# Kernel tuning notes

Hardware: AMD Instinct MI355X
Metric: run time of the kernel (lower is better)

## Reference

```python
import jax, jax.numpy as jnp
import numpy as np

BOARD_H, BOARD_W = 10, 9
NUM_NODES = BOARD_H * BOARD_W  # 90
NUM_HEADS = 4


def _build_base_adjacency():
    adj = np.zeros((NUM_NODES, NUM_NODES), dtype=np.float32)
    for y in range(BOARD_H):
        for x in range(BOARD_W):
            idx = y * BOARD_W + x
            for dy, dx in [(0, 1), (0, -1), (1, 0), (-1, 0)]:
                ny, nx = y + dy, x + dx
                if 0 <= ny < BOARD_H and 0 <= nx < BOARD_W:
                    adj[idx, ny * BOARD_W + nx] = 1.0
            for nx in range(BOARD_W):
                if nx != x and abs(nx - x) <= 4:
                    nidx = y * BOARD_W + nx
                    adj[idx, nidx] = max(adj[idx, nidx], 1.0 / abs(nx - x))
            for ny in range(BOARD_H):
                if ny != y and abs(ny - y) <= 5:
                    nidx = ny * BOARD_W + x
                    adj[idx, nidx] = max(adj[idx, nidx], 1.0 / abs(ny - y))
            adj[idx, idx] = 1.0
    deg = np.clip(adj.sum(-1, keepdims=True), 1.0, None)
    return adj / deg  # (90, 90)


def _pos_encoding():
    px = (np.arange(BOARD_W, dtype=np.float32) / BOARD_W)
    py = (np.arange(BOARD_H, dtype=np.float32) / BOARD_H)
    gx = np.broadcast_to(px[None, :], (BOARD_H, BOARD_W)).reshape(-1)
    gy = np.broadcast_to(py[:, None], (BOARD_H, BOARD_W)).reshape(-1)
    return np.stack([gx, gy], axis=-1)  # (90, 2)


def _gat_layer(x, adj, W, a_src, a_dst, gamma, beta):
    B, N, _ = x.shape
    h = (x @ W).reshape(B, N, NUM_HEADS, -1)          # (B,N,H,D)
    s_src = jnp.einsum('bnhd,hd->bhn', h, a_src)       # (B,H,N)
    s_dst = jnp.einsum('bnhd,hd->bhn', h, a_dst)
    attn = s_src[..., :, None] + s_dst[..., None, :]   # (B,H,N,N)
    attn = jax.nn.leaky_relu(attn, 0.2)
    attn = jnp.where((adj == 0)[None, None], -jnp.inf, attn)
    attn = jax.nn.softmax(attn, axis=-1)
    attn = jnp.nan_to_num(attn, nan=0.0)
    out = jnp.einsum('bhij,bjhd->bihd', attn, h).reshape(B * N, -1)
    # BatchNorm1d in training mode: biased batch stats over (B*N)
    mean = out.mean(0)
    var = out.var(0)
    out = (out - mean) * jax.lax.rsqrt(var + 1e-5) * gamma + beta
    return jax.nn.relu(out.reshape(B, N, -1))


def setup_inputs() -> dict:
    key = jax.random.key(0)
    ks = jax.random.split(key, 16)
    B, F_in, Hd, Dout = 2048, 16, 64, 128
    hdim = Hd // NUM_HEADS
    p = lambda k, s: (jax.random.normal(k, s, dtype=jnp.float32) * 0.1)
    return {
        'board_planes': jax.random.uniform(ks[0], (B, 14, BOARD_H, BOARD_W), dtype=jnp.float32),
        'in_W': p(ks[1], (F_in, Hd)), 'in_b': p(ks[2], (Hd,)),
        'W0': p(ks[3], (Hd, Hd)), 'asrc0': p(ks[4], (NUM_HEADS, hdim)), 'adst0': p(ks[5], (NUM_HEADS, hdim)),
        'g0': jnp.ones((Hd,), jnp.float32), 'b0': jnp.zeros((Hd,), jnp.float32),
        'W1': p(ks[6], (Hd, Hd)), 'asrc1': p(ks[7], (NUM_HEADS, hdim)), 'adst1': p(ks[8], (NUM_HEADS, hdim)),
        'g1': jnp.ones((Hd,), jnp.float32), 'b1': jnp.zeros((Hd,), jnp.float32),
        'out_W': p(ks[9], (Hd, Dout)), 'out_b': p(ks[10], (Dout,)),
    }


def reference(board_planes, in_W, in_b, W0, asrc0, adst0, g0, b0,
              W1, asrc1, adst1, g1, b1, out_W, out_b):
    B = board_planes.shape[0]
    adj = jnp.asarray(_build_base_adjacency())            # (90,90), same for all batches
    nodes = board_planes.reshape(B, 14, NUM_NODES).transpose(0, 2, 1)  # (B,90,14)
    pos = jnp.broadcast_to(jnp.asarray(_pos_encoding())[None], (B, NUM_NODES, 2))
    x = jnp.concatenate([nodes, pos], axis=-1)            # (B,90,16)
    x = x @ in_W + in_b
    x = _gat_layer(x, adj, W0, asrc0, adst0, g0, b0)
    x = _gat_layer(x, adj, W1, asrc1, adst1, g1, b1)
    return x.mean(axis=1) @ out_W + out_b                 # (B,128)
```

## Files before the change

### kernel.cpp

```cpp
#include <hip/hip_runtime.h>
#include <cstdint>


#define BB   2048
#define NN   90
#define NP   96
#define CC   64
#define NH   4
#define HD   16
#define TPB  512
#define DOUT 128
#define SXP  72
#define SWP  72
#define SHP  68
#define PPITCH 20
#define NSLOT 19

typedef _Float16 f16;
typedef _Float16 f16x4 __attribute__((ext_vector_type(4)));
typedef _Float16 f16x8 __attribute__((ext_vector_type(8)));
typedef float f32x4 __attribute__((ext_vector_type(4)));
union U16x4 { f16x4 v; f16 e[4]; };

#define LDS_BYTES 40832

template <int LAYER>
__global__ __launch_bounds__(TPB, 8) void k_gat(
    const float* __restrict__ bp,
    const float* __restrict__ inW,
    const float* __restrict__ inb,
    const float* __restrict__ prevPre,
    const float* __restrict__ stPrev,
    const float* __restrict__ Wl,
    const float* __restrict__ asrc,
    const float* __restrict__ adst,
    float* __restrict__ outPre,
    float* __restrict__ partial,
    float* __restrict__ partialSq)
{
    __shared__ __align__(16) unsigned char lds[LDS_BYTES];
    float* shF  = (float*)lds;
    f16*   sx   = (f16*)lds;
    f16*   sWt  = (f16*)(lds + 13824);
    unsigned char* uni = lds + 24480;
    f16*   sXr  = (f16*)uni;
    float* sInW = (float*)(uni + 3072);
    float* sInb = (float*)(uni + 7168);
    float* sAs  = (float*)(uni + 7424);
    float* sAd  = (float*)(uni + 7680);
    f16*   sPh  = (f16*)uni;
    float* sRa  = (float*)uni;
    float* sRb  = (float*)(uni + 2048);
    f16*   sSrcH = (f16*)(lds + 38880);
    f16*   sDstH = (f16*)(lds + 39600);
    float* sST   = (float*)(lds + 40320);

    const int b = blockIdx.x, t = threadIdx.x;
    const int cq = t & 15, ng = t >> 4;
    const int c4 = cq << 2;
    const int jcnt = (ng < NN - 64) ? 3 : 2;
    const int lane = t & 63, wv = t >> 6;
    const int lr = lane & 15, lg = lane >> 4;

    for (int i = t; i < CC * CC; i += TPB) {
        int k = i >> 6, c = i & 63;
        sWt[c * SWP + k] = (f16)Wl[i];
    }
    if (t < NH * HD) { sAs[t] = asrc[t]; sAd[t] = adst[t]; }
    if (t < (NP - NN) * (SXP / 4)) {
        int r = t / (SXP / 4), q = t - r * (SXP / 4);
        f16x4 z = {(f16)0, (f16)0, (f16)0, (f16)0};
        *(f16x4*)&sx[(NN + r) * SXP + q * 4] = z;
    }
    if (LAYER == 0) {
        for (int i = t; i < 16 * CC; i += TPB) sInW[i] = inW[i];
        if (t < CC) sInb[t] = inb[t];
        const float* bpb = bp + (size_t)b * (14 * NN);
        for (int i = t; i < 14 * NN; i += TPB) {
            int p = i / NN, n = i - p * NN;
            sXr[n * 17 + p] = (f16)bpb[i];
        }
        if (t < NN) {
            int y = t / 9, x = t - y * 9;
            sXr[t * 17 + 14] = (f16)((float)x / 9.0f);
            sXr[t * 17 + 15] = (f16)((float)y / 10.0f);
        }
    } else {
        if (t < 2 * CC) sST[t] = stPrev[t];
    }
    __syncthreads();

    if (LAYER == 0) {
        const int n0 = ng, n1 = ng + 32, n2 = (jcnt == 3) ? ng + 64 : ng;
        float acc[3][4] = {};
        #pragma unroll 4
        for (int k = 0; k < 16; k++) {
            float4 w = *(const float4*)&sInW[k * CC + c4];
            float x0 = (float)sXr[n0 * 17 + k];
            float x1 = (float)sXr[n1 * 17 + k];
            float x2 = (float)sXr[n2 * 17 + k];
            acc[0][0] = fmaf(x0, w.x, acc[0][0]); acc[0][1] = fmaf(x0, w.y, acc[0][1]);
            acc[0][2] = fmaf(x0, w.z, acc[0][2]); acc[0][3] = fmaf(x0, w.w, acc[0][3]);
            acc[1][0] = fmaf(x1, w.x, acc[1][0]); acc[1][1] = fmaf(x1, w.y, acc[1][1]);
            acc[1][2] = fmaf(x1, w.z, acc[1][2]); acc[1][3] = fmaf(x1, w.w, acc[1][3]);
            acc[2][0] = fmaf(x2, w.x, acc[2][0]); acc[2][1] = fmaf(x2, w.y, acc[2][1]);
            acc[2][2] = fmaf(x2, w.z, acc[2][2]); acc[2][3] = fmaf(x2, w.w, acc[2][3]);
        }
        float4 bias = *(const float4*)&sInb[c4];
        for (int j = 0; j < jcnt; j++) {
            int n = ng + 32 * j;
            f16x4 o;
            o.x = (f16)(acc[j][0] + bias.x);
            o.y = (f16)(acc[j][1] + bias.y);
            o.z = (f16)(acc[j][2] + bias.z);
            o.w = (f16)(acc[j][3] + bias.w);
            *(f16x4*)&sx[n * SXP + c4] = o;
        }
    } else {
        const float4* pv4 = (const float4*)(prevPre + (size_t)b * (NN * CC));
        for (int i4 = t; i4 < NN * CC / 4; i4 += TPB) {
            float4 v = pv4[i4];
            int n = i4 >> 4, c = (i4 & 15) << 2;
            float a0 = fmaf(v.x, sST[c + 0], sST[CC + c + 0]);
            float a1 = fmaf(v.y, sST[c + 1], sST[CC + c + 1]);
            float a2 = fmaf(v.z, sST[c + 2], sST[CC + c + 2]);
            float a3 = fmaf(v.w, sST[c + 3], sST[CC + c + 3]);
            f16x4 o;
            o.x = (f16)(a0 > 0.0f ? a0 : 0.0f);
            o.y = (f16)(a1 > 0.0f ? a1 : 0.0f);
            o.z = (f16)(a2 > 0.0f ? a2 : 0.0f);
            o.w = (f16)(a3 > 0.0f ? a3 : 0.0f);
            *(f16x4*)&sx[n * SXP + c] = o;
        }
    }
    __syncthreads();

    {
        const int nt = wv & 3, m0 = wv >> 2;
        const f16x8 bf0 = *(const f16x8*)&sWt[(nt * 16 + lr) * SWP + lg * 8];
        const f16x8 bf1 = *(const f16x8*)&sWt[(nt * 16 + lr) * SWP + 32 + lg * 8];
        f16x8 af0[3], af1[3];
        #pragma unroll
        for (int mi = 0; mi < 3; mi++) {
            const int mt = m0 + 2 * mi;
            af0[mi] = *(const f16x8*)&sx[(mt * 16 + lr) * SXP + lg * 8];
            af1[mi] = *(const f16x8*)&sx[(mt * 16 + lr) * SXP + 32 + lg * 8];
        }
        __syncthreads();
        #pragma unroll
        for (int mi = 0; mi < 3; mi++) {
            const int mt = m0 + 2 * mi;
            f32x4 acc = {0.0f, 0.0f, 0.0f, 0.0f};
            acc = __builtin_amdgcn_mfma_f32_16x16x32_f16(af0[mi], bf0, acc, 0, 0, 0);
            acc = __builtin_amdgcn_mfma_f32_16x16x32_f16(af1[mi], bf1, acc, 0, 0, 0);
            const int row = mt * 16 + lg * 4, col = nt * 16 + lr;
            #pragma unroll
            for (int r = 0; r < 4; r++)
                if (row + r < NN) shF[(row + r) * SHP + col] = acc[r];
        }
    }
    __syncthreads();

    if (t < NH * NN) {
        int hh = t / NN, n = t - hh * NN;
        const float4* hv = (const float4*)&shF[n * SHP + hh * HD];
        const float4* av = (const float4*)&sAs[hh * HD];
        const float4* dv = (const float4*)&sAd[hh * HD];
        float a = 0.0f, d = 0.0f;
        #pragma unroll
        for (int m = 0; m < 4; m++) {
            float4 h4 = hv[m], am = av[m], dm = dv[m];
            a = fmaf(h4.x, am.x, a); a = fmaf(h4.y, am.y, a);
            a = fmaf(h4.z, am.z, a); a = fmaf(h4.w, am.w, a);
            d = fmaf(h4.x, dm.x, d); d = fmaf(h4.y, dm.y, d);
            d = fmaf(h4.z, dm.z, d); d = fmaf(h4.w, dm.w, d);
        }
        sSrcH[t] = (f16)a; sDstH[t] = (f16)d;
    }
    __syncthreads();

    if (t < NH * NN) {
        int hh = t / NN, n = t - hh * NN;
        int y = n / 9, x = n - y * 9;
        float si = (float)sSrcH[t];
        float e[NSLOT];
        #pragma unroll
        for (int xx = 0; xx < 9; xx++) {
            int dx = xx > x ? xx - x : x - xx;
            float ee = si + (float)sDstH[hh * NN + y * 9 + xx];
            ee = ee > 0.0f ? ee : 0.2f * ee;
            e[xx] = (dx <= 4) ? ee : -1e30f;
        }
        #pragma unroll
        for (int yy = 0; yy < 10; yy++) {
            int dy = yy > y ? yy - y : y - yy;
            float ee = si + (float)sDstH[hh * NN + yy * 9 + x];
            ee = ee > 0.0f ? ee : 0.2f * ee;
            e[9 + yy] = (dy >= 1 && dy <= 5) ? ee : -1e30f;
        }
        float m = e[0];
        #pragma unroll
        for (int k = 1; k < NSLOT; k++) m = fmaxf(m, e[k]);
        float p[NSLOT];
        float s = 0.0f;
        #pragma unroll
        for (int k = 0; k < NSLOT; k++) { p[k] = __expf(e[k] - m); s += p[k]; }
        float inv = 1.0f / s;
        f16* pr = &sPh[t * PPITCH];
        #pragma unroll
        for (int q = 0; q < 5; q++) {
            U16x4 o;
            #pragma unroll
            for (int j = 0; j < 4; j++) {
                int k = 4 * q + j;
                o.e[j] = (k < NSLOT) ? (f16)(p[k] * inv) : (f16)0;
            }
            *(f16x4*)&pr[4 * q] = o.v;
        }
    }
    __syncthreads();

    const int hh2 = cq >> 2;
    float lsum[4] = {}, lsq[4] = {};
    float* op = outPre + (size_t)b * (NN * CC);
    for (int j = 0; j < jcnt; j++) {
        int n = ng + 32 * j;
        int y = n / 9, x = n - y * 9;
        const f16* pr = &sPh[(hh2 * NN + n) * PPITCH];
        U16x4 P0, P1, P2, P3, P4;
        P0.v = *(const f16x4*)&pr[0];
        P1.v = *(const f16x4*)&pr[4];
        P2.v = *(const f16x4*)&pr[8];
        P3.v = *(const f16x4*)&pr[12];
        P4.v = *(const f16x4*)&pr[16];
        float a0 = 0.0f, a1 = 0.0f, a2 = 0.0f, a3 = 0.0f;
        #pragma unroll
        for (int xx = 0; xx < 9; xx++) {
            float p = (xx < 4) ? (float)P0.e[xx]
                    : (xx < 8) ? (float)P1.e[xx - 4] : (float)P2.e[0];
            float4 h4 = *(const float4*)&shF[(y * 9 + xx) * SHP + c4];
            a0 = fmaf(p, h4.x, a0); a1 = fmaf(p, h4.y, a1);
            a2 = fmaf(p, h4.z, a2); a3 = fmaf(p, h4.w, a3);
        }
        #pragma unroll
        for (int yy = 0; yy < 10; yy++) {
            int k = 9 + yy;
            float p = (k < 12) ? (float)P2.e[k - 8]
                    : (k < 16) ? (float)P3.e[k - 12] : (float)P4.e[k - 16];
            float4 h4 = *(const float4*)&shF[(yy * 9 + x) * SHP + c4];
            a0 = fmaf(p, h4.x, a0); a1 = fmaf(p, h4.y, a1);
            a2 = fmaf(p, h4.z, a2); a3 = fmaf(p, h4.w, a3);
        }
        float4 o; o.x = a0; o.y = a1; o.z = a2; o.w = a3;
        *(float4*)&op[n * CC + c4] = o;
        lsum[0] += a0; lsum[1] += a1; lsum[2] += a2; lsum[3] += a3;
        lsq[0] = fmaf(a0, a0, lsq[0]); lsq[1] = fmaf(a1, a1, lsq[1]);
        lsq[2] = fmaf(a2, a2, lsq[2]); lsq[3] = fmaf(a3, a3, lsq[3]);
    }
    __syncthreads();

    #pragma unroll
    for (int q = 0; q < 4; q++) {
        float v = lsum[q];
        v += __shfl_xor(v, 16); v += __shfl_xor(v, 32);
        lsum[q] = v;
        float w2 = lsq[q];
        w2 += __shfl_xor(w2, 16); w2 += __shfl_xor(w2, 32);
        lsq[q] = w2;
    }
    if (lg == 0) {
        float4 a; a.x = lsum[0]; a.y = lsum[1]; a.z = lsum[2]; a.w = lsum[3];
        float4 c; c.x = lsq[0]; c.y = lsq[1]; c.z = lsq[2]; c.w = lsq[3];
        *(float4*)&sRa[wv * CC + c4] = a;
        *(float4*)&sRb[wv * CC + c4] = c;
    }
    __syncthreads();
    if (t < CC) {
        float s = 0.0f, q2 = 0.0f;
        #pragma unroll
        for (int g = 0; g < 8; g++) {
            s  += sRa[g * CC + t];
            q2 += sRb[g * CC + t];
        }
        partial[(size_t)b * CC + t] = s;
        partialSq[(size_t)b * CC + t] = q2;
    }
}

__global__ __launch_bounds__(256) void k_stats(
    const float* __restrict__ partial, const float* __restrict__ partialSq,
    const float* __restrict__ gamma, const float* __restrict__ beta,
    float* __restrict__ st)
{
    const int c = blockIdx.x, t = threadIdx.x;
    float s = 0.0f, q = 0.0f;
    for (int b = t; b < BB; b += 256) {
        s += partial[(size_t)b * CC + c];
        q += partialSq[(size_t)b * CC + c];
    }
    __shared__ float rs[256], rq[256];
    rs[t] = s; rq[t] = q;
    __syncthreads();
    for (int o = 128; o > 0; o >>= 1) {
        if (t < o) { rs[t] += rs[t + o]; rq[t] += rq[t + o]; }
        __syncthreads();
    }
    if (t == 0) {
        const float cntInv = 1.0f / (float)(BB * NN);
        float mean = rs[0] * cntInv;
        float var  = rq[0] * cntInv - mean * mean;
        float sc = gamma[c] * rsqrtf(var + 1e-5f);
        st[c] = sc;
        st[CC + c] = beta[c] - mean * sc;
    }
}

__global__ __launch_bounds__(256) void k_final(
    const float* __restrict__ pre, const float* __restrict__ st,
    const float* __restrict__ outW, const float* __restrict__ outb,
    float* __restrict__ out)
{
    __shared__ float sM[CC];
    __shared__ float sPart[4][CC];
    const int b = blockIdx.x, t = threadIdx.x;
    const int c = t & 63, p = t >> 6;
    const float* pv = pre + (size_t)b * (NN * CC);
    float s = st[c], sft = st[CC + c];
    float a = 0.0f;
    int nBeg = p * 23, nEnd = nBeg + 23 < NN ? nBeg + 23 : NN;
    for (int n = nBeg; n < nEnd; n++) {
        float v = fmaf(pv[n * CC + c], s, sft);
        a += (v > 0.0f ? v : 0.0f);
    }
    sPart[p][c] = a;
    __syncthreads();
    if (t < CC)
        sM[t] = (sPart[0][t] + sPart[1][t] + sPart[2][t] + sPart[3][t]) * (1.0f / (float)NN);
    __syncthreads();
    if (t < DOUT) {
        float acc = outb[t];
        #pragma unroll
        for (int cc2 = 0; cc2 < CC; cc2++) acc = fmaf(sM[cc2], outW[cc2 * DOUT + t], acc);
        out[(size_t)b * DOUT + t] = acc;
    }
}

extern "C" void kernel_launch(void* const* d_in, const int* in_sizes, int n_in,
                              void* d_out, int out_size, void* d_ws, size_t ws_size,
                              hipStream_t stream) {
    (void)in_sizes; (void)n_in; (void)out_size; (void)ws_size;

    const float* bp   = (const float*)d_in[0];
    const float* inW  = (const float*)d_in[1];
    const float* inb  = (const float*)d_in[2];
    const float* W0   = (const float*)d_in[3];
    const float* as0  = (const float*)d_in[4];
    const float* ad0  = (const float*)d_in[5];
    const float* g0   = (const float*)d_in[6];
    const float* b0   = (const float*)d_in[7];
    const float* W1   = (const float*)d_in[8];
    const float* as1  = (const float*)d_in[9];
    const float* ad1  = (const float*)d_in[10];
    const float* g1   = (const float*)d_in[11];
    const float* b1   = (const float*)d_in[12];
    const float* outW = (const float*)d_in[13];
    const float* outb = (const float*)d_in[14];
    float* out = (float*)d_out;

    float* ws = (float*)d_ws;
    float* outPre    = ws;
    float* partial   = outPre + (size_t)BB * NN * CC;
    float* partialSq = partial + (size_t)BB * CC;
    float* st0       = partialSq + (size_t)BB * CC;
    float* st1       = st0 + 2 * CC;

    k_gat<0><<<BB, TPB, 0, stream>>>(bp, inW, inb, nullptr, nullptr,
                                     W0, as0, ad0, outPre, partial, partialSq);
    k_stats<<<CC, 256, 0, stream>>>(partial, partialSq, g0, b0, st0);
    k_gat<1><<<BB, TPB, 0, stream>>>(nullptr, nullptr, nullptr, outPre, st0,
                                     W1, as1, ad1, outPre, partial, partialSq);
    k_stats<<<CC, 256, 0, stream>>>(partial, partialSq, g1, b1, st1);
    k_final<<<BB, 256, 0, stream>>>(outPre, st1, outW, outb, out);
}
```

Baseline: 125.7 us.

## Use MFMA for input projection and store projected features as fp16 in LDS

Replaces the scalar FMA input projection in layer 0 with a single 16x16x32 MFMA per tile, using zero-padded fp16 input and transposed weight buffers. Projected node features are now kept as fp16 in LDS instead of fp32, so each aggregation thread handles 8 channels per 16-byte load. Attention scores stay in fp32. The LDS layout is reorganised, the BatchNorm partial-sum reduction becomes a two-stage LDS reduction, and launch bounds drop from 8 to 6 blocks per CU. The fp16 feature storage lowers precision, and the larger LDS footprint may reduce occupancy.

```diff
diff --git a/kernel.cpp b/kernel.cpp
--- a/kernel.cpp
+++ b/kernel.cpp
@@ -12,20 +12,22 @@
 #define DOUT 128
 #define SXP  72
 #define SWP  72
-#define SHP  68
+#define XRP  32
 #define PPITCH 20
+#define RPITCH 68
 #define NSLOT 19
 
 typedef _Float16 f16;
 typedef _Float16 f16x4 __attribute__((ext_vector_type(4)));
 typedef _Float16 f16x8 __attribute__((ext_vector_type(8)));
 typedef float f32x4 __attribute__((ext_vector_type(4)));
+union U16x8 { f16x8 v; f16 e[8]; };
 union U16x4 { f16x4 v; f16 e[4]; };
 
-#define LDS_BYTES 40832
+#define LDS_BYTES 41216
 
 template <int LAYER>
-__global__ __launch_bounds__(TPB, 8) void k_gat(
+__global__ __launch_bounds__(TPB, 6) void k_gat(
     const float* __restrict__ bp,
     const float* __restrict__ inW,
     const float* __restrict__ inb,
@@ -39,26 +41,24 @@
     float* __restrict__ partialSq)
 {
     __shared__ __align__(16) unsigned char lds[LDS_BYTES];
-    float* shF  = (float*)lds;
-    f16*   sx   = (f16*)lds;
-    f16*   sWt  = (f16*)(lds + 13824);
-    unsigned char* uni = lds + 24480;
-    f16*   sXr  = (f16*)uni;
-    float* sInW = (float*)(uni + 3072);
-    float* sInb = (float*)(uni + 7168);
-    float* sAs  = (float*)(uni + 7424);
-    float* sAd  = (float*)(uni + 7680);
-    f16*   sPh  = (f16*)uni;
-    float* sRa  = (float*)uni;
-    float* sRb  = (float*)(uni + 2048);
-    f16*   sSrcH = (f16*)(lds + 38880);
-    f16*   sDstH = (f16*)(lds + 39600);
-    float* sST   = (float*)(lds + 40320);
+    f16*   sx    = (f16*)lds;
+    f16*   sh16  = (f16*)lds;
+    f16*   sWt   = (f16*)(lds + 13824);
+    f16*   sXr   = (f16*)(lds + 23040);
+    f16*   sInWt = (f16*)(lds + 29184);
+    float* sInb  = (float*)(lds + 33280);
+    float* sAs   = (float*)(lds + 33536);
+    float* sAd   = (float*)(lds + 33792);
+    f16*   sPh   = (f16*)(lds + 13824);
+    float* sSrc  = (float*)(lds + 34816);
+    float* sDst  = (float*)(lds + 36256);
+    float* sST   = (float*)(lds + 37696);
+    float* sRa   = (float*)lds;
+    float* sRb   = (float*)(lds + 17408);
+    float* sP2a  = (float*)(lds + 34816);
+    float* sP2b  = (float*)(lds + 36864);
 
     const int b = blockIdx.x, t = threadIdx.x;
-    const int cq = t & 15, ng = t >> 4;
-    const int c4 = cq << 2;
-    const int jcnt = (ng < NN - 64) ? 3 : 2;
     const int lane = t & 63, wv = t >> 6;
     const int lr = lane & 15, lg = lane >> 4;
 
@@ -67,54 +67,48 @@
         sWt[c * SWP + k] = (f16)Wl[i];
     }
     if (t < NH * HD) { sAs[t] = asrc[t]; sAd[t] = adst[t]; }
-    if (t < (NP - NN) * (SXP / 4)) {
-        int r = t / (SXP / 4), q = t - r * (SXP / 4);
-        f16x4 z = {(f16)0, (f16)0, (f16)0, (f16)0};
-        *(f16x4*)&sx[(NN + r) * SXP + q * 4] = z;
-    }
     if (LAYER == 0) {
-        for (int i = t; i < 16 * CC; i += TPB) sInW[i] = inW[i];
-        if (t < CC) sInb[t] = inb[t];
-        const float* bpb = bp + (size_t)b * (14 * NN);
         for (int i = t; i < 14 * NN; i += TPB) {
-            int p = i / NN, n = i - p * NN;
-            sXr[n * 17 + p] = (f16)bpb[i];
+            int n = i / 14, p = i - n * 14;
+            sXr[n * XRP + p] = (f16)bp[(size_t)b * (14 * NN) + p * NN + n];
         }
         if (t < NN) {
             int y = t / 9, x = t - y * 9;
-            sXr[t * 17 + 14] = (f16)((float)x / 9.0f);
-            sXr[t * 17 + 15] = (f16)((float)y / 10.0f);
-        }
+            sXr[t * XRP + 14] = (f16)((float)x / 9.0f);
+            sXr[t * XRP + 15] = (f16)((float)y / 10.0f);
+        }
+        if (t < NP * 2) {
+            f16x8 z = {};
+            *(f16x8*)&sXr[(t >> 1) * XRP + 16 + (t & 1) * 8] = z;
+        }
+        for (int i = t; i < 16 * CC; i += TPB) {
+            int c = i >> 4, k = i & 15;
+            sInWt[c * XRP + k] = (f16)inW[k * CC + c];
+        }
+        if (t < CC * 2) {
+            f16x8 z = {};
+            *(f16x8*)&sInWt[(t >> 1) * XRP + 16 + (t & 1) * 8] = z;
+        }
+        if (t < CC) sInb[t] = inb[t];
     } else {
         if (t < 2 * CC) sST[t] = stPrev[t];
     }
     __syncthreads();
 
     if (LAYER == 0) {
-        const int n0 = ng, n1 = ng + 32, n2 = (jcnt == 3) ? ng + 64 : ng;
-        float acc[3][4] = {};
-        #pragma unroll 4
-        for (int k = 0; k < 16; k++) {
-            float4 w = *(const float4*)&sInW[k * CC + c4];
-            float x0 = (float)sXr[n0 * 17 + k];
-            float x1 = (float)sXr[n1 * 17 + k];
-            float x2 = (float)sXr[n2 * 17 + k];
-            acc[0][0] = fmaf(x0, w.x, acc[0][0]); acc[0][1] = fmaf(x0, w.y, acc[0][1]);
-            acc[0][2] = fmaf(x0, w.z, acc[0][2]); acc[0][3] = fmaf(x0, w.w, acc[0][3]);
-            acc[1][0] = fmaf(x1, w.x, acc[1][0]); acc[1][1] = fmaf(x1, w.y, acc[1][1]);
-            acc[1][2] = fmaf(x1, w.z, acc[1][2]); acc[1][3] = fmaf(x1, w.w, acc[1][3]);
-            acc[2][0] = fmaf(x2, w.x, acc[2][0]); acc[2][1] = fmaf(x2, w.y, acc[2][1]);
-            acc[2][2] = fmaf(x2, w.z, acc[2][2]); acc[2][3] = fmaf(x2, w.w, acc[2][3]);
-        }
-        float4 bias = *(const float4*)&sInb[c4];
-        for (int j = 0; j < jcnt; j++) {
-            int n = ng + 32 * j;
-            f16x4 o;
-            o.x = (f16)(acc[j][0] + bias.x);
-            o.y = (f16)(acc[j][1] + bias.y);
-            o.z = (f16)(acc[j][2] + bias.z);
-            o.w = (f16)(acc[j][3] + bias.w);
-            *(f16x4*)&sx[n * SXP + c4] = o;
+        const int nt = wv & 3, m0 = wv >> 2;
+        const f16x8 bf = *(const f16x8*)&sInWt[(nt * 16 + lr) * XRP + lg * 8];
+        const float bias = sInb[nt * 16 + lr];
+        #pragma unroll
+        for (int mi = 0; mi < 3; mi++) {
+            const int mt = m0 + 2 * mi;
+            const f16x8 af = *(const f16x8*)&sXr[(mt * 16 + lr) * XRP + lg * 8];
+            f32x4 acc = {0.0f, 0.0f, 0.0f, 0.0f};
+            acc = __builtin_amdgcn_mfma_f32_16x16x32_f16(af, bf, acc, 0, 0, 0);
+            const int row = mt * 16 + lg * 4, col = nt * 16 + lr;
+            #pragma unroll
+            for (int r = 0; r < 4; r++)
+                sx[(row + r) * SXP + col] = (f16)(acc[r] + bias);
         }
     } else {
         const float4* pv4 = (const float4*)(prevPre + (size_t)b * (NN * CC));
@@ -156,45 +150,44 @@
             const int row = mt * 16 + lg * 4, col = nt * 16 + lr;
             #pragma unroll
             for (int r = 0; r < 4; r++)
-                if (row + r < NN) shF[(row + r) * SHP + col] = acc[r];
+                sh16[(row + r) * SXP + col] = (f16)acc[r];
         }
     }
     __syncthreads();
 
     if (t < NH * NN) {
         int hh = t / NN, n = t - hh * NN;
-        const float4* hv = (const float4*)&shF[n * SHP + hh * HD];
-        const float4* av = (const float4*)&sAs[hh * HD];
-        const float4* dv = (const float4*)&sAd[hh * HD];
+        U16x8 h0, h1;
+        h0.v = *(const f16x8*)&sh16[n * SXP + hh * HD];
+        h1.v = *(const f16x8*)&sh16[n * SXP + hh * HD + 8];
         float a = 0.0f, d = 0.0f;
         #pragma unroll
-        for (int m = 0; m < 4; m++) {
-            float4 h4 = hv[m], am = av[m], dm = dv[m];
-            a = fmaf(h4.x, am.x, a); a = fmaf(h4.y, am.y, a);
-            a = fmaf(h4.z, am.z, a); a = fmaf(h4.w, am.w, a);
-            d = fmaf(h4.x, dm.x, d); d = fmaf(h4.y, dm.y, d);
-            d = fmaf(h4.z, dm.z, d); d = fmaf(h4.w, dm.w, d);
-        }
-        sSrcH[t] = (f16)a; sDstH[t] = (f16)d;
+        for (int j = 0; j < 8; j++) {
+            a = fmaf((float)h0.e[j], sAs[hh * HD + j], a);
+            a = fmaf((float)h1.e[j], sAs[hh * HD + 8 + j], a);
+            d = fmaf((float)h0.e[j], sAd[hh * HD + j], d);
+            d = fmaf((float)h1.e[j], sAd[hh * HD + 8 + j], d);
+        }
+        sSrc[t] = a; sDst[t] = d;
     }
     __syncthreads();
 
     if (t < NH * NN) {
         int hh = t / NN, n = t - hh * NN;
         int y = n / 9, x = n - y * 9;
-        float si = (float)sSrcH[t];
+        float si = sSrc[t];
         float e[NSLOT];
         #pragma unroll
         for (int xx = 0; xx < 9; xx++) {
             int dx = xx > x ? xx - x : x - xx;
-            float ee = si + (float)sDstH[hh * NN + y * 9 + xx];
+            float ee = si + sDst[hh * NN + y * 9 + xx];
             ee = ee > 0.0f ? ee : 0.2f * ee;
             e[xx] = (dx <= 4) ? ee : -1e30f;
         }
         #pragma unroll
         for (int yy = 0; yy < 10; yy++) {
             int dy = yy > y ? yy - y : y - yy;
-            float ee = si + (float)sDstH[hh * NN + yy * 9 + x];
+            float ee = si + sDst[hh * NN + yy * 9 + x];
             ee = ee > 0.0f ? ee : 0.2f * ee;
             e[9 + yy] = (dy >= 1 && dy <= 5) ? ee : -1e30f;
         }
@@ -220,70 +213,86 @@
     }
     __syncthreads();
 
-    const int hh2 = cq >> 2;
-    float lsum[4] = {}, lsq[4] = {};
+    const int c8i = t & 7, nr = t >> 3;
+    const int ch = c8i << 3, hh6 = c8i >> 1;
+    const int nrows = (nr < NN - 64) ? 2 : 1;
+    float lsum[8] = {}, lsq[8] = {};
     float* op = outPre + (size_t)b * (NN * CC);
-    for (int j = 0; j < jcnt; j++) {
-        int n = ng + 32 * j;
+    for (int j = 0; j < nrows; j++) {
+        int n = nr + 64 * j;
         int y = n / 9, x = n - y * 9;
-        const f16* pr = &sPh[(hh2 * NN + n) * PPITCH];
+        const f16* pr = &sPh[(hh6 * NN + n) * PPITCH];
         U16x4 P0, P1, P2, P3, P4;
         P0.v = *(const f16x4*)&pr[0];
         P1.v = *(const f16x4*)&pr[4];
         P2.v = *(const f16x4*)&pr[8];
         P3.v = *(const f16x4*)&pr[12];
         P4.v = *(const f16x4*)&pr[16];
-        float a0 = 0.0f, a1 = 0.0f, a2 = 0.0f, a3 = 0.0f;
+        float a[8] = {};
         #pragma unroll
         for (int xx = 0; xx < 9; xx++) {
             float p = (xx < 4) ? (float)P0.e[xx]
                     : (xx < 8) ? (float)P1.e[xx - 4] : (float)P2.e[0];
-            float4 h4 = *(const float4*)&shF[(y * 9 + xx) * SHP + c4];
-            a0 = fmaf(p, h4.x, a0); a1 = fmaf(p, h4.y, a1);
-            a2 = fmaf(p, h4.z, a2); a3 = fmaf(p, h4.w, a3);
+            U16x8 h8; h8.v = *(const f16x8*)&sh16[(y * 9 + xx) * SXP + ch];
+            #pragma unroll
+            for (int q = 0; q < 8; q++) a[q] = fmaf((float)h8.e[q], p, a[q]);
         }
         #pragma unroll
         for (int yy = 0; yy < 10; yy++) {
             int k = 9 + yy;
             float p = (k < 12) ? (float)P2.e[k - 8]
                     : (k < 16) ? (float)P3.e[k - 12] : (float)P4.e[k - 16];
-            float4 h4 = *(const float4*)&shF[(yy * 9 + x) * SHP + c4];
-            a0 = fmaf(p, h4.x, a0); a1 = fmaf(p, h4.y, a1);
-            a2 = fmaf(p, h4.z, a2); a3 = fmaf(p, h4.w, a3);
-        }
-        float4 o; o.x = a0; o.y = a1; o.z = a2; o.w = a3;
-        *(float4*)&op[n * CC + c4] = o;
-        lsum[0] += a0; lsum[1] += a1; lsum[2] += a2; lsum[3] += a3;
-        lsq[0] = fmaf(a0, a0, lsq[0]); lsq[1] = fmaf(a1, a1, lsq[1]);
-        lsq[2] = fmaf(a2, a2, lsq[2]); lsq[3] = fmaf(a3, a3, lsq[3]);
-    }
-    __syncthreads();
-
-    #pragma unroll
-    for (int q = 0; q < 4; q++) {
-        float v = lsum[q];
-        v += __shfl_xor(v, 16); v += __shfl_xor(v, 32);
-        lsum[q] = v;
-        float w2 = lsq[q];
-        w2 += __shfl_xor(w2, 16); w2 += __shfl_xor(w2, 32);
-        lsq[q] = w2;
-    }
-    if (lg == 0) {
-        float4 a; a.x = lsum[0]; a.y = lsum[1]; a.z = lsum[2]; a.w = lsum[3];
-        float4 c; c.x = lsq[0]; c.y = lsq[1]; c.z = lsq[2]; c.w = lsq[3];
-        *(float4*)&sRa[wv * CC + c4] = a;
-        *(float4*)&sRb[wv * CC + c4] = c;
+            U16x8 h8; h8.v = *(const f16x8*)&sh16[(yy * 9 + x) * SXP + ch];
+            #pragma unroll
+            for (int q = 0; q < 8; q++) a[q] = fmaf((float)h8.e[q], p, a[q]);
+        }
+        float4 o1, o2;
+        o1.x = a[0]; o1.y = a[1]; o1.z = a[2]; o1.w = a[3];
+        o2.x = a[4]; o2.y = a[5]; o2.z = a[6]; o2.w = a[7];
+        *(float4*)&op[n * CC + ch] = o1;
+        *(float4*)&op[n * CC + ch + 4] = o2;
+        #pragma unroll
+        for (int q = 0; q < 8; q++) {
+            lsum[q] += a[q];
+            lsq[q] = fmaf(a[q], a[q], lsq[q]);
+        }
+    }
+    __syncthreads();
+
+    {
+        float4 w1, w2;
+        w1.x = lsum[0]; w1.y = lsum[1]; w1.z = lsum[2]; w1.w = lsum[3];
+        w2.x = lsum[4]; w2.y = lsum[5]; w2.z = lsum[6]; w2.w = lsum[7];
+        *(float4*)&sRa[nr * RPITCH + ch] = w1;
+        *(float4*)&sRa[nr * RPITCH + ch + 4] = w2;
+        w1.x = lsq[0]; w1.y = lsq[1]; w1.z = lsq[2]; w1.w = lsq[3];
+        w2.x = lsq[4]; w2.y = lsq[5]; w2.z = lsq[6]; w2.w = lsq[7];
+        *(float4*)&sRb[nr * RPITCH + ch] = w1;
+        *(float4*)&sRb[nr * RPITCH + ch + 4] = w2;
+    }
+    __syncthreads();
+    {
+        const int c = t & 63, part = t >> 6;
+        float s = 0.0f, q = 0.0f;
+        #pragma unroll
+        for (int g = 0; g < 8; g++) {
+            int row = part + 8 * g;
+            s += sRa[row * RPITCH + c];
+            q += sRb[row * RPITCH + c];
+        }
+        sP2a[part * CC + c] = s;
+        sP2b[part * CC + c] = q;
     }
     __syncthreads();
     if (t < CC) {
-        float s = 0.0f, q2 = 0.0f;
-        #pragma unroll
-        for (int g = 0; g < 8; g++) {
-            s  += sRa[g * CC + t];
-            q2 += sRb[g * CC + t];
+        float s = 0.0f, q = 0.0f;
+        #pragma unroll
+        for (int p = 0; p < 8; p++) {
+            s += sP2a[p * CC + t];
+            q += sP2b[p * CC + t];
         }
         partial[(size_t)b * CC + t] = s;
-        partialSq[(size_t)b * CC + t] = q2;
+        partialSq[(size_t)b * CC + t] = q;
     }
 }
 
```

After: 172.0 us. 1.37x slower.

## Store inter-layer activations and projected features in fp16, restructure LDS

Applied to the files above, without the earlier changes.

Stores the intermediate pre-BatchNorm activations in global memory as fp16 instead of fp32, which halves the write/read traffic between the two GAT kernels and the final kernel. The projected node features in LDS also become fp16, sharing the input buffer, while the attention scores stay fp32. The LDS layout is split into separate arrays, the batch-stat reduction drops shuffles in favour of 32 LDS partial rows, and launch bounds go from 8 to 6 waves per SIMD. Precision drops for the stored activations, and the statistics are computed on the rounded values.

```diff
diff --git a/kernel.cpp b/kernel.cpp
--- a/kernel.cpp
+++ b/kernel.cpp
@@ -12,7 +12,6 @@
 #define DOUT 128
 #define SXP  72
 #define SWP  72
-#define SHP  68
 #define PPITCH 20
 #define NSLOT 19
 
@@ -21,39 +20,38 @@
 typedef _Float16 f16x8 __attribute__((ext_vector_type(8)));
 typedef float f32x4 __attribute__((ext_vector_type(4)));
 union U16x4 { f16x4 v; f16 e[4]; };
-
-#define LDS_BYTES 40832
+union U16x8 { f16x8 v; f16 e[8]; };
+
 
 template <int LAYER>
-__global__ __launch_bounds__(TPB, 8) void k_gat(
+__global__ __launch_bounds__(TPB, 6) void k_gat(
     const float* __restrict__ bp,
     const float* __restrict__ inW,
     const float* __restrict__ inb,
-    const float* __restrict__ prevPre,
+    const f16*   __restrict__ prevPre,
     const float* __restrict__ stPrev,
     const float* __restrict__ Wl,
     const float* __restrict__ asrc,
     const float* __restrict__ adst,
-    float* __restrict__ outPre,
+    f16*   __restrict__ outPre,
     float* __restrict__ partial,
     float* __restrict__ partialSq)
 {
-    __shared__ __align__(16) unsigned char lds[LDS_BYTES];
-    float* shF  = (float*)lds;
-    f16*   sx   = (f16*)lds;
-    f16*   sWt  = (f16*)(lds + 13824);
-    unsigned char* uni = lds + 24480;
-    f16*   sXr  = (f16*)uni;
-    float* sInW = (float*)(uni + 3072);
-    float* sInb = (float*)(uni + 7168);
-    float* sAs  = (float*)(uni + 7424);
-    float* sAd  = (float*)(uni + 7680);
+    __shared__ __align__(16) unsigned char big[13824];
+    __shared__ __align__(16) unsigned char uni[19712];
+    __shared__ float sAs[NH * HD], sAd[NH * HD];
+    __shared__ float sSrc[NH][NN], sDst[NH][NN];
+    __shared__ float sST[2 * CC];
+
+    f16*   sx   = (f16*)big;
+    f16*   sh16 = (f16*)big;
+    f16*   sWt  = (f16*)uni;
+    float* sInW = (float*)(uni + 9216);
+    float* sInb = (float*)(uni + 13312);
+    float* sXr  = (float*)(uni + 13568);
     f16*   sPh  = (f16*)uni;
     float* sRa  = (float*)uni;
-    float* sRb  = (float*)(uni + 2048);
-    f16*   sSrcH = (f16*)(lds + 38880);
-    f16*   sDstH = (f16*)(lds + 39600);
-    float* sST   = (float*)(lds + 40320);
+    float* sRb  = (float*)(uni + 8192);
 
     const int b = blockIdx.x, t = threadIdx.x;
     const int cq = t & 15, ng = t >> 4;
@@ -78,12 +76,12 @@
         const float* bpb = bp + (size_t)b * (14 * NN);
         for (int i = t; i < 14 * NN; i += TPB) {
             int p = i / NN, n = i - p * NN;
-            sXr[n * 17 + p] = (f16)bpb[i];
+            sXr[n * 17 + p] = bpb[i];
         }
         if (t < NN) {
             int y = t / 9, x = t - y * 9;
-            sXr[t * 17 + 14] = (f16)((float)x / 9.0f);
-            sXr[t * 17 + 15] = (f16)((float)y / 10.0f);
+            sXr[t * 17 + 14] = (float)x / 9.0f;
+            sXr[t * 17 + 15] = (float)y / 10.0f;
         }
     } else {
         if (t < 2 * CC) sST[t] = stPrev[t];
@@ -96,9 +94,7 @@
         #pragma unroll 4
         for (int k = 0; k < 16; k++) {
             float4 w = *(const float4*)&sInW[k * CC + c4];
-            float x0 = (float)sXr[n0 * 17 + k];
-            float x1 = (float)sXr[n1 * 17 + k];
-            float x2 = (float)sXr[n2 * 17 + k];
+            float x0 = sXr[n0 * 17 + k], x1 = sXr[n1 * 17 + k], x2 = sXr[n2 * 17 + k];
             acc[0][0] = fmaf(x0, w.x, acc[0][0]); acc[0][1] = fmaf(x0, w.y, acc[0][1]);
             acc[0][2] = fmaf(x0, w.z, acc[0][2]); acc[0][3] = fmaf(x0, w.w, acc[0][3]);
             acc[1][0] = fmaf(x1, w.x, acc[1][0]); acc[1][1] = fmaf(x1, w.y, acc[1][1]);
@@ -117,20 +113,17 @@
             *(f16x4*)&sx[n * SXP + c4] = o;
         }
     } else {
-        const float4* pv4 = (const float4*)(prevPre + (size_t)b * (NN * CC));
-        for (int i4 = t; i4 < NN * CC / 4; i4 += TPB) {
-            float4 v = pv4[i4];
-            int n = i4 >> 4, c = (i4 & 15) << 2;
-            float a0 = fmaf(v.x, sST[c + 0], sST[CC + c + 0]);
-            float a1 = fmaf(v.y, sST[c + 1], sST[CC + c + 1]);
-            float a2 = fmaf(v.z, sST[c + 2], sST[CC + c + 2]);
-            float a3 = fmaf(v.w, sST[c + 3], sST[CC + c + 3]);
-            f16x4 o;
-            o.x = (f16)(a0 > 0.0f ? a0 : 0.0f);
-            o.y = (f16)(a1 > 0.0f ? a1 : 0.0f);
-            o.z = (f16)(a2 > 0.0f ? a2 : 0.0f);
-            o.w = (f16)(a3 > 0.0f ? a3 : 0.0f);
-            *(f16x4*)&sx[n * SXP + c] = o;
+        const f16x8* pv8 = (const f16x8*)(prevPre + (size_t)b * (NN * CC));
+        for (int i8 = t; i8 < NN * CC / 8; i8 += TPB) {
+            U16x8 v; v.v = pv8[i8];
+            int n = i8 >> 3, c8 = (i8 & 7) << 3;
+            U16x8 o;
+            #pragma unroll
+            for (int j = 0; j < 8; j++) {
+                float a = fmaf((float)v.e[j], sST[c8 + j], sST[CC + c8 + j]);
+                o.e[j] = (f16)(a > 0.0f ? a : 0.0f);
+            }
+            *(f16x8*)&sx[n * SXP + c8] = o.v;
         }
     }
     __syncthreads();
@@ -156,45 +149,44 @@
             const int row = mt * 16 + lg * 4, col = nt * 16 + lr;
             #pragma unroll
             for (int r = 0; r < 4; r++)
-                if (row + r < NN) shF[(row + r) * SHP + col] = acc[r];
+                sh16[(row + r) * SXP + col] = (f16)acc[r];
         }
     }
     __syncthreads();
 
     if (t < NH * NN) {
         int hh = t / NN, n = t - hh * NN;
-        const float4* hv = (const float4*)&shF[n * SHP + hh * HD];
-        const float4* av = (const float4*)&sAs[hh * HD];
-        const float4* dv = (const float4*)&sAd[hh * HD];
+        U16x8 h0, h1;
+        h0.v = *(const f16x8*)&sh16[n * SXP + hh * HD];
+        h1.v = *(const f16x8*)&sh16[n * SXP + hh * HD + 8];
         float a = 0.0f, d = 0.0f;
         #pragma unroll
-        for (int m = 0; m < 4; m++) {
-            float4 h4 = hv[m], am = av[m], dm = dv[m];
-            a = fmaf(h4.x, am.x, a); a = fmaf(h4.y, am.y, a);
-            a = fmaf(h4.z, am.z, a); a = fmaf(h4.w, am.w, a);
-            d = fmaf(h4.x, dm.x, d); d = fmaf(h4.y, dm.y, d);
-            d = fmaf(h4.z, dm.z, d); d = fmaf(h4.w, dm.w, d);
-        }
-        sSrcH[t] = (f16)a; sDstH[t] = (f16)d;
+        for (int j = 0; j < 8; j++) {
+            a = fmaf((float)h0.e[j], sAs[hh * HD + j], a);
+            a = fmaf((float)h1.e[j], sAs[hh * HD + 8 + j], a);
+            d = fmaf((float)h0.e[j], sAd[hh * HD + j], d);
+            d = fmaf((float)h1.e[j], sAd[hh * HD + 8 + j], d);
+        }
+        sSrc[hh][n] = a; sDst[hh][n] = d;
     }
     __syncthreads();
 
     if (t < NH * NN) {
         int hh = t / NN, n = t - hh * NN;
         int y = n / 9, x = n - y * 9;
-        float si = (float)sSrcH[t];
+        float si = sSrc[hh][n];
         float e[NSLOT];
         #pragma unroll
         for (int xx = 0; xx < 9; xx++) {
             int dx = xx > x ? xx - x : x - xx;
-            float ee = si + (float)sDstH[hh * NN + y * 9 + xx];
+            float ee = si + sDst[hh][y * 9 + xx];
             ee = ee > 0.0f ? ee : 0.2f * ee;
             e[xx] = (dx <= 4) ? ee : -1e30f;
         }
         #pragma unroll
         for (int yy = 0; yy < 10; yy++) {
             int dy = yy > y ? yy - y : y - yy;
-            float ee = si + (float)sDstH[hh * NN + yy * 9 + x];
+            float ee = si + sDst[hh][yy * 9 + x];
             ee = ee > 0.0f ? ee : 0.2f * ee;
             e[9 + yy] = (dy >= 1 && dy <= 5) ? ee : -1e30f;
         }
@@ -222,7 +214,7 @@
 
     const int hh2 = cq >> 2;
     float lsum[4] = {}, lsq[4] = {};
-    float* op = outPre + (size_t)b * (NN * CC);
+    f16* op = outPre + (size_t)b * (NN * CC);
     for (int j = 0; j < jcnt; j++) {
         int n = ng + 32 * j;
         int y = n / 9, x = n - y * 9;
@@ -238,47 +230,40 @@
         for (int xx = 0; xx < 9; xx++) {
             float p = (xx < 4) ? (float)P0.e[xx]
                     : (xx < 8) ? (float)P1.e[xx - 4] : (float)P2.e[0];
-            float4 h4 = *(const float4*)&shF[(y * 9 + xx) * SHP + c4];
-            a0 = fmaf(p, h4.x, a0); a1 = fmaf(p, h4.y, a1);
-            a2 = fmaf(p, h4.z, a2); a3 = fmaf(p, h4.w, a3);
+            U16x4 h4; h4.v = *(const f16x4*)&sh16[(y * 9 + xx) * SXP + c4];
+            a0 = fmaf((float)h4.e[0], p, a0); a1 = fmaf((float)h4.e[1], p, a1);
+            a2 = fmaf((float)h4.e[2], p, a2); a3 = fmaf((float)h4.e[3], p, a3);
         }
         #pragma unroll
         for (int yy = 0; yy < 10; yy++) {
             int k = 9 + yy;
             float p = (k < 12) ? (float)P2.e[k - 8]
                     : (k < 16) ? (float)P3.e[k - 12] : (float)P4.e[k - 16];
-            float4 h4 = *(const float4*)&shF[(yy * 9 + x) * SHP + c4];
-            a0 = fmaf(p, h4.x, a0); a1 = fmaf(p, h4.y, a1);
-            a2 = fmaf(p, h4.z, a2); a3 = fmaf(p, h4.w, a3);
-        }
-        float4 o; o.x = a0; o.y = a1; o.z = a2; o.w = a3;
-        *(float4*)&op[n * CC + c4] = o;
-        lsum[0] += a0; lsum[1] += a1; lsum[2] += a2; lsum[3] += a3;
-        lsq[0] = fmaf(a0, a0, lsq[0]); lsq[1] = fmaf(a1, a1, lsq[1]);
-        lsq[2] = fmaf(a2, a2, lsq[2]); lsq[3] = fmaf(a3, a3, lsq[3]);
+            U16x4 h4; h4.v = *(const f16x4*)&sh16[(yy * 9 + x) * SXP + c4];
+            a0 = fmaf((float)h4.e[0], p, a0); a1 = fmaf((float)h4.e[1], p, a1);
+            a2 = fmaf((float)h4.e[2], p, a2); a3 = fmaf((float)h4.e[3], p, a3);
+        }
+        U16x4 o;
+        o.e[0] = (f16)a0; o.e[1] = (f16)a1; o.e[2] = (f16)a2; o.e[3] = (f16)a3;
+        *(f16x4*)&op[n * CC + c4] = o.v;
+        float r0 = (float)o.e[0], r1 = (float)o.e[1];
+        float r2 = (float)o.e[2], r3 = (float)o.e[3];
+        lsum[0] += r0; lsum[1] += r1; lsum[2] += r2; lsum[3] += r3;
+        lsq[0] = fmaf(r0, r0, lsq[0]); lsq[1] = fmaf(r1, r1, lsq[1]);
+        lsq[2] = fmaf(r2, r2, lsq[2]); lsq[3] = fmaf(r3, r3, lsq[3]);
     }
     __syncthreads();
 
     #pragma unroll
     for (int q = 0; q < 4; q++) {
-        float v = lsum[q];
-        v += __shfl_xor(v, 16); v += __shfl_xor(v, 32);
-        lsum[q] = v;
-        float w2 = lsq[q];
-        w2 += __shfl_xor(w2, 16); w2 += __shfl_xor(w2, 32);
-        lsq[q] = w2;
-    }
-    if (lg == 0) {
-        float4 a; a.x = lsum[0]; a.y = lsum[1]; a.z = lsum[2]; a.w = lsum[3];
-        float4 c; c.x = lsq[0]; c.y = lsq[1]; c.z = lsq[2]; c.w = lsq[3];
-        *(float4*)&sRa[wv * CC + c4] = a;
-        *(float4*)&sRb[wv * CC + c4] = c;
+        sRa[ng * CC + c4 + q] = lsum[q];
+        sRb[ng * CC + c4 + q] = lsq[q];
     }
     __syncthreads();
     if (t < CC) {
         float s = 0.0f, q2 = 0.0f;
         #pragma unroll
-        for (int g = 0; g < 8; g++) {
+        for (int g = 0; g < 32; g++) {
             s  += sRa[g * CC + t];
             q2 += sRb[g * CC + t];
         }
@@ -316,7 +301,7 @@
 }
 
 __global__ __launch_bounds__(256) void k_final(
-    const float* __restrict__ pre, const float* __restrict__ st,
+    const f16* __restrict__ pre, const float* __restrict__ st,
     const float* __restrict__ outW, const float* __restrict__ outb,
     float* __restrict__ out)
 {
@@ -324,12 +309,12 @@
     __shared__ float sPart[4][CC];
     const int b = blockIdx.x, t = threadIdx.x;
     const int c = t & 63, p = t >> 6;
-    const float* pv = pre + (size_t)b * (NN * CC);
+    const f16* pv = pre + (size_t)b * (NN * CC);
     float s = st[c], sft = st[CC + c];
     float a = 0.0f;
     int nBeg = p * 23, nEnd = nBeg + 23 < NN ? nBeg + 23 : NN;
     for (int n = nBeg; n < nEnd; n++) {
-        float v = fmaf(pv[n * CC + c], s, sft);
+        float v = fmaf((float)pv[n * CC + c], s, sft);
         a += (v > 0.0f ? v : 0.0f);
     }
     sPart[p][c] = a;
@@ -367,11 +352,11 @@
     const float* outb = (const float*)d_in[14];
     float* out = (float*)d_out;
 
-    float* ws = (float*)d_ws;
-    float* outPre    = ws;
-    float* partial   = outPre + (size_t)BB * NN * CC;
-    float* partialSq = partial + (size_t)BB * CC;
-    float* st0       = partialSq + (size_t)BB * CC;
+    unsigned char* ws = (unsigned char*)d_ws;
+    f16*   outPre    = (f16*)ws;
+    float* partial   = (float*)(ws + 23592960);
+    float* partialSq = (float*)(ws + 23592960 + 524288);
+    float* st0       = (float*)(ws + 23592960 + 1048576);
     float* st1       = st0 + 2 * CC;
 
     k_gat<0><<<BB, TPB, 0, stream>>>(bp, inW, inb, nullptr, nullptr,
```

Measured after the change: 111.0 us (median of 2 runs). -11.7%, faster.
